# Kernel tuning notes

Hardware: AMD Instinct MI355X
Metric: run time of the kernel (lower is better)

## Reference

```python
import jax, jax.numpy as jnp
import numpy as np

N = 500000   # total nodes in batched graph
B = 8192     # number of graphs
H = 128      # hidden_dim
L = 3        # num_layer -> feature_dim F = H*L = 384
F = H * L
S2S_STEPS = 3
VOCAB = 143


def setup_inputs() -> dict:
    key = jax.random.key(0)
    ks = jax.random.split(key, 12)
    sc = 0.02
    unit_type = jax.random.randint(ks[0], (N,), 0, VOCAB)
    # sorted segment ids covering every graph (contiguous, all B segments non-empty)
    node2graph = (jnp.arange(N) * B) // N
    return {
        'unit_type': unit_type,
        'node2graph': node2graph,
        'embed':    jax.random.normal(ks[1], (VOCAB, H)) * sc,
        'msg_W1':   jax.random.normal(ks[2], (H, 2 * H)) * sc,
        'msg_b1':   jnp.zeros((H,)),
        'msg_W2':   jax.random.normal(ks[3], (H, H)) * sc,
        'msg_b2':   jnp.zeros((H,)),
        'gru_Wih':  jax.random.normal(ks[4], (3 * H, H)) * sc,
        'gru_Whh':  jax.random.normal(ks[5], (3 * H, H)) * sc,
        'gru_bih':  jnp.zeros((3 * H,)),
        'gru_bhh':  jnp.zeros((3 * H,)),
        'lstm_Wih': jax.random.normal(ks[6], (4 * F, 2 * F)) * sc,
        'lstm_Whh': jax.random.normal(ks[7], (4 * F, F)) * sc,
        'lstm_bih': jnp.zeros((4 * F,)),
        'lstm_bhh': jnp.zeros((4 * F,)),
    }


def _gru_step(x, h, Wih, Whh, bih, bhh):
    # single-timestep PyTorch GRU cell; gate order r, z, n
    gi = x @ Wih.T + bih
    gh = h @ Whh.T + bhh
    ir, iz, inn = jnp.split(gi, 3, axis=-1)
    hr, hz, hn = jnp.split(gh, 3, axis=-1)
    r = jax.nn.sigmoid(ir + hr)
    z = jax.nn.sigmoid(iz + hz)
    n = jnp.tanh(inn + r * hn)
    return (1.0 - z) * n + z * h


def _lstm_step(x, h, c, Wih, Whh, bih, bhh):
    # single-timestep PyTorch LSTM cell; gate order i, f, g, o
    g = x @ Wih.T + bih + h @ Whh.T + bhh
    i, f, gc, o = jnp.split(g, 4, axis=-1)
    c = jax.nn.sigmoid(f) * c + jax.nn.sigmoid(i) * jnp.tanh(gc)
    h = jax.nn.sigmoid(o) * jnp.tanh(c)
    return h, c


def reference(unit_type, node2graph, embed, msg_W1, msg_b1, msg_W2, msg_b2,
              gru_Wih, gru_Whh, gru_bih, gru_bhh,
              lstm_Wih, lstm_Whh, lstm_bih, lstm_bhh):
    # --- node update stack ---
    layer_input = embed[unit_type]          # [N, H]
    hx = layer_input                        # GRU hidden state (1 layer)
    hiddens = []
    for _ in range(L):
        x2 = jnp.concatenate([layer_input, layer_input], axis=-1)   # [N, 2H]
        msg = jnp.maximum(x2 @ msg_W1.T + msg_b1, 0.0) @ msg_W2.T + msg_b2
        hx = _gru_step(msg, hx, gru_Wih, gru_Whh, gru_bih, gru_bhh)
        hiddens.append(hx)
        layer_input = hx
    node_feature = jnp.concatenate(hiddens, axis=-1)                # [N, F]

    # --- Set2Set readout ---
    h = jnp.zeros((B, F), dtype=node_feature.dtype)
    c = jnp.zeros((B, F), dtype=node_feature.dtype)
    q_star = jnp.zeros((B, 2 * F), dtype=node_feature.dtype)
    for _ in range(S2S_STEPS):
        h, c = _lstm_step(q_star, h, c, lstm_Wih, lstm_Whh, lstm_bih, lstm_bhh)
        q = h                                                       # [B, F]
        logits = jnp.sum(q[node2graph] * node_feature, axis=-1)     # [N]
        m = jax.ops.segment_max(logits, node2graph, num_segments=B,
                                indices_are_sorted=True)
        e = jnp.exp(logits - m[node2graph])
        z = jax.ops.segment_sum(e, node2graph, num_segments=B,
                                indices_are_sorted=True)
        att = e / z[node2graph]                                     # [N]
        pooled = jax.ops.segment_sum(att[:, None] * node_feature, node2graph,
                                     num_segments=B, indices_are_sorted=True)
        q_star = jnp.concatenate([q, pooled], axis=-1)              # [B, 2F]

    return q_star, node_feature
```

## Files before the change

### kernel.cpp

```cpp
#include <hip/hip_runtime.h>

typedef unsigned short u16;
typedef unsigned int   u32;
typedef u16 bfx8 __attribute__((ext_vector_type(8)));
typedef __bf16 bf16x8 __attribute__((ext_vector_type(8)));
typedef float  f32x4  __attribute__((ext_vector_type(4)));

#define NH  128
#define NF  384
#define K2F 768
#define NG4 1536

__device__ __forceinline__ float bf2f(u16 u){ return __uint_as_float(((u32)u) << 16); }
__device__ __forceinline__ u16 f2bf(float f){
  u32 x = __float_as_uint(f);
  u32 r = x + 0x7fffu + ((x >> 16) & 1u);
  return (u16)(r >> 16);
}
__device__ __forceinline__ float fsig(float x){ return 1.0f / (1.0f + __expf(-x)); }
__device__ __forceinline__ float ftanh(float x){ return 1.0f - 2.0f / (__expf(2.0f * x) + 1.0f); }

struct P {
  const int *unit_type, *n2g;
  const void *embed, *w1, *b1, *w2, *b2, *gwih, *gwhh, *gbih, *gbhh, *lwih, *lwhh, *lbih, *lbhh;
  int *flag, *segS, *segE;
  u16 *W1eb, *W2b, *Wihb, *Whhb;
  float *b1f, *b2f, *bihG, *bhhG;
  float *Wcat;
  float *bsum;
  float *h1v, *c1v;
  float *hbuf, *cbuf, *pooled;
  float *xcat;
  float *gout;
  u16 *nfb;
  int useNfb;
  void *out; long qsz;
  int N, B, embedN;
};

__device__ __forceinline__ float ldin(const void* p, long i, int isbf){
  return isbf ? bf2f(((const u16*)p)[i]) : ((const float*)p)[i];
}

__global__ void k_detect(P p){
  __shared__ int cnt;
  if (threadIdx.x == 0) cnt = 0;
  __syncthreads();
  const u32* w = (const u32*)p.embed;
  const int nw = p.embedN / 2;
  int bad = 0;
  for (int i = threadIdx.x; i < nw; i += blockDim.x){
    u32 v = w[i];
    float fhi = __uint_as_float(v & 0xffff0000u);
    float flo = __uint_as_float(v << 16);
    if (!(fabsf(fhi) < 2.0f)) bad++;
    if (!(fabsf(flo) < 2.0f)) bad++;
  }
  atomicAdd(&cnt, bad);
  __syncthreads();
  if (threadIdx.x == 0) *p.flag = (cnt == 0) ? 1 : 0;
}

__global__ void k_prep(P p){
  long o = (long)blockIdx.x * 256 + threadIdx.x;
  const int isbf = *p.flag;
  if (o < 16384){ long cc = o >> 7, k = o & 127;
    float v = ldin(p.w1, cc*256 + k, isbf) + ldin(p.w1, cc*256 + 128 + k, isbf);
    p.W1eb[o] = f2bf(v); return; } o -= 16384;
  if (o < 16384){ p.W2b[o]  = f2bf(ldin(p.w2, o, isbf));   return; } o -= 16384;
  if (o < 49152){ p.Wihb[o] = f2bf(ldin(p.gwih, o, isbf)); return; } o -= 49152;
  if (o < 49152){ p.Whhb[o] = f2bf(ldin(p.gwhh, o, isbf)); return; } o -= 49152;
  if (o < (long)NG4*K2F){ long j = o / K2F, k = o - j*K2F;
    float v = ldin(p.lwih, o, isbf);
    if (k < NF) v += ldin(p.lwhh, j*NF + k, isbf);
    p.Wcat[o] = v; return; } o -= (long)NG4*K2F;
  if (o < NH){ p.b1f[o] = ldin(p.b1, o, isbf); return; } o -= NH;
  if (o < NH){ p.b2f[o] = ldin(p.b2, o, isbf); return; } o -= NH;
  if (o < NF){ p.bihG[o] = ldin(p.gbih, o, isbf); return; } o -= NF;
  if (o < NF){ p.bhhG[o] = ldin(p.gbhh, o, isbf); return; } o -= NF;
  if (o < NG4){ p.bsum[o] = ldin(p.lbih, o, isbf) + ldin(p.lbhh, o, isbf); return; } o -= NG4;
  if (o < p.B){ p.segS[o] = 0; p.segE[o] = 0; }
}

__global__ void k_segb(P p){
  int i = (int)blockIdx.x * 256 + threadIdx.x;
  if (i >= p.N) return;
  int g = p.n2g[i];
  if (g < 0 || g >= p.B) return;
  if (i == 0        || p.n2g[i-1] != g) p.segS[g] = i;
  if (i == p.N - 1  || p.n2g[i+1] != g) p.segE[g] = i + 1;
}

__device__ __forceinline__ f32x4 MF(bf16x8 a, bf16x8 b, f32x4 c){
  return __builtin_amdgcn_mfma_f32_16x16x32_bf16(a, b, c, 0, 0, 0);
}
__device__ __forceinline__ bf16x8 ldA(const u16* buf, int m0, int k0, int lane){
  const int row = m0 + (lane & 15);
  const int byte = (row*256 + (k0 + (lane>>4)*8)*2) ^ ((row&7)<<4);
  return *(const bf16x8*)((const char*)buf + byte);
}
__device__ __forceinline__ bf16x8 ldB(const u16* __restrict__ W, int n0, int k0, int lane){
  return *(const bf16x8*)(W + (long)(n0 + (lane&15))*NH + k0 + (lane>>4)*8);
}
__device__ __forceinline__ void stLDS(u16* buf, int row, int col, float v){
  const int byte = (row*256 + col*2) ^ ((row&7)<<4);
  *(u16*)((char*)buf + byte) = f2bf(v);
}
__device__ __forceinline__ void stLDSu(u16* buf, int row, int col, u16 v){
  const int byte = (row*256 + col*2) ^ ((row&7)<<4);
  *(u16*)((char*)buf + byte) = v;
}
__device__ __forceinline__ float ldLDS(const u16* buf, int row, int col){
  const int byte = (row*256 + col*2) ^ ((row&7)<<4);
  return bf2f(*(const u16*)((const char*)buf + byte));
}
__device__ __forceinline__ bfx8 ldLDS8(const u16* buf, int row, int col8){
  const int byte = (row*256 + col8*2) ^ ((row&7)<<4);
  return *(const bfx8*)((const char*)buf + byte);
}

__global__ __launch_bounds__(256, 3) void k_stageA_mfma(P p){
  __shared__ u16 hA[64*128];
  __shared__ u16 mA[64*128];
  __shared__ u16 gA[64*128];
  const int t = (int)threadIdx.x;
  const int lane = t & 63, w = t >> 6;
  const int node0 = (int)blockIdx.x * 64;
  const int cL = lane & 15;
  const int isbf = *p.flag;

  u16 st[2][2][4][4];

  {
    const int row = t >> 2, seg = t & 3;
    const int node = min(node0 + row, p.N - 1);
    int ut = p.unit_type[node];
    ut = min(max(ut, 0), p.embedN/NH - 1);
    if (isbf){
      const u16* src = (const u16*)p.embed + (long)ut*NH + seg*32;
      #pragma unroll
      for (int i = 0; i < 4; ++i){
        const int col = seg*32 + i*8;
        const int byte = (row*256 + col*2) ^ ((row&7)<<4);
        *(bfx8*)((char*)hA + byte) = *(const bfx8*)(src + i*8);
      }
    } else {
      const float* src = (const float*)p.embed + (long)ut*NH + seg*32;
      #pragma unroll
      for (int i = 0; i < 4; ++i){
        const int col = seg*32 + i*8;
        u16 tmp[8];
        #pragma unroll
        for (int j = 0; j < 8; ++j) tmp[j] = f2bf(src[i*8 + j]);
        const int byte = (row*256 + col*2) ^ ((row&7)<<4);
        *(bfx8*)((char*)hA + byte) = *(const bfx8*)tmp;
      }
    }
  }
  __syncthreads();

  u16*   out16 = (u16*)p.out;
  float* out32 = (float*)p.out;

  #pragma unroll 1
  for (int l = 0; l < 3; ++l){
    {
      f32x4 acc[2][4];
      #pragma unroll
      for (int nt = 0; nt < 2; ++nt){
        const float b = p.b1f[w*32 + nt*16 + cL];
        #pragma unroll
        for (int m = 0; m < 4; ++m) acc[nt][m] = {b,b,b,b};
      }
      for (int k0 = 0; k0 < 128; k0 += 32){
        bf16x8 a[4];
        #pragma unroll
        for (int m = 0; m < 4; ++m) a[m] = ldA(hA, m*16, k0, lane);
        #pragma unroll
        for (int nt = 0; nt < 2; ++nt){
          const bf16x8 b = ldB(p.W1eb, w*32 + nt*16, k0, lane);
          #pragma unroll
          for (int m = 0; m < 4; ++m) acc[nt][m] = MF(a[m], b, acc[nt][m]);
        }
      }
      #pragma unroll
      for (int nt = 0; nt < 2; ++nt)
        #pragma unroll
        for (int m = 0; m < 4; ++m)
          #pragma unroll
          for (int j = 0; j < 4; ++j)
            stLDS(mA, m*16 + (lane>>4)*4 + j, w*32 + nt*16 + cL,
                  fmaxf(acc[nt][m][j], 0.0f));
    }
    __syncthreads();
    {
      f32x4 acc[2][4];
      #pragma unroll
      for (int nt = 0; nt < 2; ++nt){
        const float b = p.b2f[w*32 + nt*16 + cL];
        #pragma unroll
        for (int m = 0; m < 4; ++m) acc[nt][m] = {b,b,b,b};
      }
      for (int k0 = 0; k0 < 128; k0 += 32){
        bf16x8 a[4];
        #pragma unroll
        for (int m = 0; m < 4; ++m) a[m] = ldA(mA, m*16, k0, lane);
        #pragma unroll
        for (int nt = 0; nt < 2; ++nt){
          const bf16x8 b = ldB(p.W2b, w*32 + nt*16, k0, lane);
          #pragma unroll
          for (int m = 0; m < 4; ++m) acc[nt][m] = MF(a[m], b, acc[nt][m]);
        }
      }
      __syncthreads();
      #pragma unroll
      for (int nt = 0; nt < 2; ++nt)
        #pragma unroll
        for (int m = 0; m < 4; ++m)
          #pragma unroll
          for (int j = 0; j < 4; ++j)
            stLDS(gA, m*16 + (lane>>4)*4 + j, w*32 + nt*16 + cL, acc[nt][m][j]);
    }
    __syncthreads();
    f32x4 rr[2][4];
    {
      f32x4 acc[4][4];
      #pragma unroll
      for (int tc = 0; tc < 4; ++tc){
        const int col = (tc < 2 ? 0 : 128) + w*32 + (tc&1)*16 + cL;
        const float b = p.bihG[col] + p.bhhG[col];
        #pragma unroll
        for (int m = 0; m < 4; ++m) acc[tc][m] = {b,b,b,b};
      }
      for (int k0 = 0; k0 < 128; k0 += 32){
        bf16x8 a[4];
        #pragma unroll
        for (int m = 0; m < 4; ++m) a[m] = ldA(gA, m*16, k0, lane);
        #pragma unroll
        for (int tc = 0; tc < 4; ++tc){
          const bf16x8 b = ldB(p.Wihb, (tc < 2 ? 0 : 128) + w*32 + (tc&1)*16, k0, lane);
          #pragma unroll
          for (int m = 0; m < 4; ++m) acc[tc][m] = MF(a[m], b, acc[tc][m]);
        }
      }
      for (int k0 = 0; k0 < 128; k0 += 32){
        bf16x8 a[4];
        #pragma unroll
        for (int m = 0; m < 4; ++m) a[m] = ldA(hA, m*16, k0, lane);
        #pragma unroll
        for (int tc = 0; tc < 4; ++tc){
          const bf16x8 b = ldB(p.Whhb, (tc < 2 ? 0 : 128) + w*32 + (tc&1)*16, k0, lane);
          #pragma unroll
          for (int m = 0; m < 4; ++m) acc[tc][m] = MF(a[m], b, acc[tc][m]);
        }
      }
      #pragma unroll
      for (int nt = 0; nt < 2; ++nt)
        #pragma unroll
        for (int m = 0; m < 4; ++m)
          #pragma unroll
          for (int j = 0; j < 4; ++j){
            rr[nt][m][j] = fsig(acc[nt][m][j]);
            stLDS(mA, m*16 + (lane>>4)*4 + j, w*32 + nt*16 + cL,
                  fsig(acc[nt+2][m][j]));
          }
    }
    {
      f32x4 inn[2][4], hnn[2][4];
      #pragma unroll
      for (int nt = 0; nt < 2; ++nt){
        const int col = 256 + w*32 + nt*16 + cL;
        const float bi = p.bihG[col], bh = p.bhhG[col];
        #pragma unroll
        for (int m = 0; m < 4; ++m){ inn[nt][m] = {bi,bi,bi,bi}; hnn[nt][m] = {bh,bh,bh,bh}; }
      }
      for (int k0 = 0; k0 < 128; k0 += 32){
        bf16x8 a[4];
        #pragma unroll
        for (int m = 0; m < 4; ++m) a[m] = ldA(gA, m*16, k0, lane);
        #pragma unroll
        for (int nt = 0; nt < 2; ++nt){
          const bf16x8 b = ldB(p.Wihb, 256 + w*32 + nt*16, k0, lane);
          #pragma unroll
          for (int m = 0; m < 4; ++m) inn[nt][m] = MF(a[m], b, inn[nt][m]);
        }
      }
      for (int k0 = 0; k0 < 128; k0 += 32){
        bf16x8 a[4];
        #pragma unroll
        for (int m = 0; m < 4; ++m) a[m] = ldA(hA, m*16, k0, lane);
        #pragma unroll
        for (int nt = 0; nt < 2; ++nt){
          const bf16x8 b = ldB(p.Whhb, 256 + w*32 + nt*16, k0, lane);
          #pragma unroll
          for (int m = 0; m < 4; ++m) hnn[nt][m] = MF(a[m], b, hnn[nt][m]);
        }
      }
      #pragma unroll
      for (int nt = 0; nt < 2; ++nt)
        #pragma unroll
        for (int m = 0; m < 4; ++m)
          #pragma unroll
          for (int j = 0; j < 4; ++j){
            const int row = m*16 + (lane>>4)*4 + j;
            const int col = w*32 + nt*16 + cL;
            const float nn = ftanh(fmaf(rr[nt][m][j], hnn[nt][m][j], inn[nt][m][j]));
            const float zv = ldLDS(mA, row, col);
            const float hv = ldLDS(hA, row, col);
            inn[nt][m][j] = fmaf(zv, hv - nn, nn);
          }
      __syncthreads();
      #pragma unroll
      for (int nt = 0; nt < 2; ++nt)
        #pragma unroll
        for (int m = 0; m < 4; ++m)
          #pragma unroll
          for (int j = 0; j < 4; ++j){
            const u16 hv16 = f2bf(inn[nt][m][j]);
            stLDSu(hA, m*16 + (lane>>4)*4 + j, w*32 + nt*16 + cL, hv16);
            if (l == 0) st[0][nt][m][j] = hv16;
            else if (l == 1) st[1][nt][m][j] = hv16;
          }
      __syncthreads();
    }
  }

  #pragma unroll
  for (int nt = 0; nt < 2; ++nt)
    #pragma unroll
    for (int m = 0; m < 4; ++m)
      #pragma unroll
      for (int j = 0; j < 4; ++j){
        const int row = m*16 + (lane>>4)*4 + j;
        const int col = w*32 + nt*16 + cL;
        stLDSu(mA, row, col, st[0][nt][m][j]);
        stLDSu(gA, row, col, st[1][nt][m][j]);
      }
  __syncthreads();

  {
    const int r0 = t >> 4;
    const int c8 = (t & 15) * 8;
    #pragma unroll
    for (int r4 = 0; r4 < 4; ++r4){
      const int row = r0 + r4*16;
      const int node = node0 + row;
      if (node < p.N){
        const bfx8 v0 = ldLDS8(mA, row, c8);
        const bfx8 v1 = ldLDS8(gA, row, c8);
        const bfx8 v2 = ldLDS8(hA, row, c8);
        const long base = (long)node*NF;
        if (isbf){
          __builtin_nontemporal_store(v0, (bfx8*)(out16 + p.qsz + base + c8));
          __builtin_nontemporal_store(v1, (bfx8*)(out16 + p.qsz + base + NH + c8));
          __builtin_nontemporal_store(v2, (bfx8*)(out16 + p.qsz + base + 2*NH + c8));
        } else {
          #pragma unroll
          for (int lyr = 0; lyr < 3; ++lyr){
            const bfx8 v = lyr == 0 ? v0 : (lyr == 1 ? v1 : v2);
            f32x4 lo, hi;
            #pragma unroll
            for (int j = 0; j < 4; ++j){ lo[j] = bf2f(v[j]); hi[j] = bf2f(v[j+4]); }
            __builtin_nontemporal_store(lo, (f32x4*)(out32 + p.qsz + base + lyr*NH + c8));
            __builtin_nontemporal_store(hi, (f32x4*)(out32 + p.qsz + base + lyr*NH + c8 + 4));
          }
          if (p.useNfb){
            __builtin_nontemporal_store(v0, (bfx8*)(p.nfb + base + c8));
            __builtin_nontemporal_store(v1, (bfx8*)(p.nfb + base + NH + c8));
            __builtin_nontemporal_store(v2, (bfx8*)(p.nfb + base + 2*NH + c8));
          }
        }
      }
    }
  }
}

__global__ void k_lstm0(P p){
  const int d = (int)threadIdx.x;
  if (d >= NF) return;
  const float i_ = fsig(p.bsum[d]);
  const float gc = ftanh(p.bsum[2*NF + d]);
  const float o_ = fsig(p.bsum[3*NF + d]);
  const float cn = i_ * gc;
  p.c1v[d] = cn;
  p.h1v[d] = o_ * ftanh(cn);
}

__global__ __launch_bounds__(256) void k_attn(P p, const float* __restrict__ qsrc,
                                              int qstride, int finalstep){
  __shared__ alignas(16) char raw[32 * NF * 4];
  __shared__ float qs[NF];
  __shared__ float att[32];
  __shared__ float sM, sZ, sSc;

  u16*   nb = (u16*)raw;
  float* nfl = (float*)raw;
  const int t = (int)threadIdx.x;
  const int g = (int)blockIdx.x;
  const int isbf = *p.flag;
  const int bftile = isbf | p.useNfb;
  const u16* nbase = isbf ? (const u16*)p.out + p.qsz : p.nfb;
  const float* o32 = (const float*)p.out;

  for (int i = t; i < NF; i += 256) qs[i] = qsrc[(long)g*qstride + i];
  if (t == 0){ sM = -1e30f; sZ = 0.0f; sSc = 1.0f; }
  int n0 = p.segS[g], n1 = p.segE[g];
  n0 = max(n0, 0); n1 = min(n1, p.N);
  float acc0 = 0.f, acc1 = 0.f;
  __syncthreads();

  for (int base = n0; base < n1; base += 32){
    const int cnt = min(32, n1 - base);
    {
      const int i = t >> 3, q8 = t & 7;
      if (i < cnt){
        if (bftile){
          const bfx8* src = (const bfx8*)(nbase + (long)(base + i)*NF + q8*48);
          #pragma unroll
          for (int j8 = 0; j8 < 6; ++j8)
            *(bfx8*)&nb[i*NF + q8*48 + j8*8] = __builtin_nontemporal_load(src + j8);
        } else {
          const f32x4* src = (const f32x4*)(o32 + p.qsz + (long)(base + i)*NF + q8*48);
          #pragma unroll
          for (int j4 = 0; j4 < 12; ++j4)
            *(f32x4*)&nfl[i*NF + q8*48 + j4*4] = __builtin_nontemporal_load(src + j4);
        }
      }
    }
    __syncthreads();
    {
      const int w = t >> 6, lane = t & 63;
      for (int ii = w; ii < cnt; ii += 4){
        float dot = 0.f;
        #pragma unroll
        for (int j = 0; j < 6; ++j){
          const int d = lane + 64*j;
          const float v = bftile ? bf2f(nb[ii*NF + d]) : nfl[ii*NF + d];
          dot = fmaf(v, qs[d], dot);
        }
        #pragma unroll
        for (int off = 32; off; off >>= 1) dot += __shfl_xor(dot, off);
        if (lane == 0) att[ii] = dot;
      }
    }
    __syncthreads();
    if (t < 32){
      const float l = (t < cnt) ? att[t] : -1e30f;
      float m = l;
      #pragma unroll
      for (int off = 16; off; off >>= 1) m = fmaxf(m, __shfl_xor(m, off));
      const float mnew = fmaxf(sM, m);
      const float e = (t < cnt) ? __expf(l - mnew) : 0.f;
      float z = e;
      #pragma unroll
      for (int off = 16; off; off >>= 1) z += __shfl_xor(z, off);
      if (t < cnt) att[t] = e;
      if (t == 0){
        const float sc = __expf(sM - mnew);
        sSc = sc; sZ = sZ * sc + z; sM = mnew;
      }
    }
    __syncthreads();
    {
      const float sc = sSc;
      acc0 *= sc; acc1 *= sc;
      for (int ii = 0; ii < cnt; ++ii){
        const float a = att[ii];
        const float v0 = bftile ? bf2f(nb[ii*NF + t]) : nfl[ii*NF + t];
        acc0 = fmaf(a, v0, acc0);
        if (t < 128){
          const float v1 = bftile ? bf2f(nb[ii*NF + 256 + t]) : nfl[ii*NF + 256 + t];
          acc1 = fmaf(a, v1, acc1);
        }
      }
    }
    __syncthreads();
  }

  const float invZ = (sZ != 0.0f) ? 1.0f / sZ : 0.0f;
  const float p0 = acc0 * invZ, p1 = acc1 * invZ;
  p.pooled[(long)g*NF + t] = p0;
  if (t < 128) p.pooled[(long)g*NF + 256 + t] = p1;
  if (finalstep){
    const long rb = (long)g * K2F;
    if (isbf){
      u16* o = (u16*)p.out;
      o[rb + t] = f2bf(qs[t]);
      if (t < 128) o[rb + 256 + t] = f2bf(qs[256 + t]);
      o[rb + NF + t] = f2bf(p0);
      if (t < 128) o[rb + NF + 256 + t] = f2bf(p1);
    } else {
      float* o = (float*)p.out;
      o[rb + t] = qs[t];
      if (t < 128) o[rb + 256 + t] = qs[256 + t];
      o[rb + NF + t] = p0;
      if (t < 128) o[rb + NF + 256 + t] = p1;
    }
  }
}

__global__ void k_xcat(P p, const float* __restrict__ hsrc, int hstride){
  const int d2 = (int)blockIdx.x * 256 + threadIdx.x;
  const int g  = (int)blockIdx.y;
  if (d2 >= K2F) return;
  const float v = (d2 < NF) ? hsrc[(long)g*hstride + d2]
                            : p.pooled[(long)g*NF + d2 - NF];
  p.xcat[(long)g*K2F + d2] = v;
}

__global__ __launch_bounds__(256) void k_gemm(P p){
  __shared__ alignas(16) float aT[32][128];
  __shared__ alignas(16) float wT[32][128];
  const int t = (int)threadIdx.x;
  const int tx = t & 15, ty = t >> 4;
  const int row0 = (int)blockIdx.x * 128, col0 = (int)blockIdx.y * 128;
  const int M = p.B;
  float acc[8][8];
  #pragma unroll
  for (int i = 0; i < 8; ++i)
    #pragma unroll
    for (int j = 0; j < 8; ++j) acc[i][j] = 0.f;

  const int r = t >> 1, ks = (t & 1) * 16;
  for (int kc = 0; kc < K2F; kc += 32){
    {
      const int gr = row0 + r;
      float v[16];
      if (gr < M){
        const float* src = p.xcat + (long)gr*K2F + kc + ks;
        *(float4*)&v[0]  = *(const float4*)(src);
        *(float4*)&v[4]  = *(const float4*)(src + 4);
        *(float4*)&v[8]  = *(const float4*)(src + 8);
        *(float4*)&v[12] = *(const float4*)(src + 12);
      } else {
        #pragma unroll
        for (int j = 0; j < 16; ++j) v[j] = 0.f;
      }
      #pragma unroll
      for (int j = 0; j < 16; ++j) aT[ks+j][r] = v[j];
      const float* wsrc = p.Wcat + (long)(col0 + r)*K2F + kc + ks;
      *(float4*)&v[0]  = *(const float4*)(wsrc);
      *(float4*)&v[4]  = *(const float4*)(wsrc + 4);
      *(float4*)&v[8]  = *(const float4*)(wsrc + 8);
      *(float4*)&v[12] = *(const float4*)(wsrc + 12);
      #pragma unroll
      for (int j = 0; j < 16; ++j) wT[ks+j][r] = v[j];
    }
    __syncthreads();
    #pragma unroll 2
    for (int k = 0; k < 32; ++k){
      float a[8], wv[8];
      *(float4*)&a[0]  = *(const float4*)&aT[k][ty*8];
      *(float4*)&a[4]  = *(const float4*)&aT[k][ty*8 + 4];
      *(float4*)&wv[0] = *(const float4*)&wT[k][tx*8];
      *(float4*)&wv[4] = *(const float4*)&wT[k][tx*8 + 4];
      #pragma unroll
      for (int i = 0; i < 8; ++i)
        #pragma unroll
        for (int j = 0; j < 8; ++j) acc[i][j] = fmaf(a[i], wv[j], acc[i][j]);
    }
    __syncthreads();
  }
  float bs[8];
  #pragma unroll
  for (int j = 0; j < 8; ++j) bs[j] = p.bsum[col0 + tx*8 + j];
  #pragma unroll
  for (int i = 0; i < 8; ++i){
    const int gr = row0 + ty*8 + i;
    if (gr < M){
      float* crow = p.gout + (long)gr*NG4 + col0 + tx*8;
      float o[8];
      #pragma unroll
      for (int j = 0; j < 8; ++j) o[j] = acc[i][j] + bs[j];
      *(float4*)&crow[0] = *(const float4*)&o[0];
      *(float4*)&crow[4] = *(const float4*)&o[4];
    }
  }
}

__global__ void k_gates(P p, const float* __restrict__ csrc, int cstride){
  const long idx = (long)blockIdx.x * 256 + threadIdx.x;
  if (idx >= (long)p.B * NF) return;
  const int g = (int)(idx / NF), d = (int)(idx - (long)g*NF);
  const float* gr = p.gout + (long)g*NG4;
  const float i_ = fsig(gr[d]);
  const float f_ = fsig(gr[NF + d]);
  const float gc = ftanh(gr[2*NF + d]);
  const float o_ = fsig(gr[3*NF + d]);
  const float cp = csrc[(long)g*cstride + d];
  const float cn = fmaf(f_, cp, i_ * gc);
  p.cbuf[(long)g*NF + d] = cn;
  p.hbuf[(long)g*NF + d] = o_ * ftanh(cn);
}

extern "C" void kernel_launch(void* const* d_in, const int* in_sizes, int n_in,
                              void* d_out, int out_size, void* d_ws, size_t ws_size,
                              hipStream_t stream){
  P p{};
  p.unit_type = (const int*)d_in[0];
  p.n2g  = (const int*)d_in[1];
  p.embed = d_in[2];  p.w1 = d_in[3];  p.b1 = d_in[4];  p.w2 = d_in[5];  p.b2 = d_in[6];
  p.gwih = d_in[7];  p.gwhh = d_in[8]; p.gbih = d_in[9]; p.gbhh = d_in[10];
  p.lwih = d_in[11]; p.lwhh = d_in[12]; p.lbih = d_in[13]; p.lbhh = d_in[14];

  const int N = in_sizes[0];
  const int B = (int)(((long)out_size - (long)N*NF) / K2F);
  p.N = N; p.B = B; p.embedN = in_sizes[2];
  p.out = d_out; p.qsz = (long)B * K2F;

  char* w = (char*)d_ws;
  size_t used = 0;
  auto alloc = [&](size_t bytes) -> char* {
    char* r = w + used;
    used += (bytes + 255) & ~(size_t)255;
    return r;
  };
  p.flag  = (int*)alloc(4);
  p.segS  = (int*)alloc((size_t)B*4);
  p.segE  = (int*)alloc((size_t)B*4);
  p.W1eb  = (u16*)  alloc(16384*2);
  p.W2b   = (u16*)  alloc(16384*2);
  p.Wihb  = (u16*)  alloc(49152*2);
  p.Whhb  = (u16*)  alloc(49152*2);
  p.b1f   = (float*)alloc(NH*4);
  p.b2f   = (float*)alloc(NH*4);
  p.bihG  = (float*)alloc(NF*4);
  p.bhhG  = (float*)alloc(NF*4);
  p.Wcat  = (float*)alloc((size_t)NG4*K2F*4);
  p.bsum  = (float*)alloc(NG4*4);
  p.h1v   = (float*)alloc(NF*4);
  p.c1v   = (float*)alloc(NF*4);
  p.hbuf  = (float*)alloc((size_t)B*NF*4);
  p.cbuf  = (float*)alloc((size_t)B*NF*4);
  p.pooled= (float*)alloc((size_t)B*NF*4);
  p.xcat  = (float*)alloc((size_t)B*K2F*4);
  p.gout  = (float*)alloc((size_t)B*NG4*4);
  if (used > ws_size){
    (void)hipMemsetAsync(d_out, 0, (size_t)out_size * 2, stream);
    return;
  }
  const size_t nfbBytes = (size_t)N * NF * 2;
  if (used + nfbBytes + 256 <= ws_size){
    p.nfb = (u16*)alloc(nfbBytes);
    p.useNfb = 1;
  } else {
    p.nfb = (u16*)p.flag;
    p.useNfb = 0;
  }

  const long prepTot = 16384 + 16384 + 49152 + 49152
                     + (long)NG4*K2F + NH + NH + NF + NF + NG4 + B;

  k_detect<<<1, 256, 0, stream>>>(p);
  k_prep  <<<(int)((prepTot + 255)/256), 256, 0, stream>>>(p);
  k_segb  <<<(N + 255)/256, 256, 0, stream>>>(p);
  k_stageA_mfma<<<(N + 63)/64, 256, 0, stream>>>(p);
  k_lstm0 <<<1, NF, 0, stream>>>(p);

  const int gemmGx = (B + 127)/128;
  k_attn <<<B, 256, 0, stream>>>(p, p.h1v, 0, 0);
  k_xcat <<<dim3(3, B), 256, 0, stream>>>(p, p.h1v, 0);
  k_gemm <<<dim3(gemmGx, NG4/128), 256, 0, stream>>>(p);
  k_gates<<<(int)(((long)B*NF + 255)/256), 256, 0, stream>>>(p, p.c1v, 0);
  k_attn <<<B, 256, 0, stream>>>(p, p.hbuf, NF, 0);
  k_xcat <<<dim3(3, B), 256, 0, stream>>>(p, p.hbuf, NF);
  k_gemm <<<dim3(gemmGx, NG4/128), 256, 0, stream>>>(p);
  k_gates<<<(int)(((long)B*NF + 255)/256), 256, 0, stream>>>(p, p.cbuf, NF);
  k_attn <<<B, 256, 0, stream>>>(p, p.hbuf, NF, 1);
}
```

Before: 2.373 ms.

## Cut stage-A LDS and registers to raise occupancy, store layers incrementally

```diff
diff --git a/kernel.cpp b/kernel.cpp
--- a/kernel.cpp
+++ b/kernel.cpp
@@ -3,6 +3,7 @@
 typedef unsigned short u16;
 typedef unsigned int   u32;
 typedef u16 bfx8 __attribute__((ext_vector_type(8)));
+typedef u16 bfx4 __attribute__((ext_vector_type(4)));
 typedef __bf16 bf16x8 __attribute__((ext_vector_type(8)));
 typedef float  f32x4  __attribute__((ext_vector_type(4)));
 
@@ -24,6 +25,7 @@
   const int *unit_type, *n2g;
   const void *embed, *w1, *b1, *w2, *b2, *gwih, *gwhh, *gbih, *gbhh, *lwih, *lwhh, *lbih, *lbhh;
   int *flag, *segS, *segE;
+  u16 *embedB;
   u16 *W1eb, *W2b, *Wihb, *Whhb;
   float *b1f, *b2f, *bihG, *bhhG;
   float *Wcat;
@@ -64,6 +66,7 @@
 __global__ void k_prep(P p){
   long o = (long)blockIdx.x * 256 + threadIdx.x;
   const int isbf = *p.flag;
+  if (o < p.embedN){ p.embedB[o] = f2bf(ldin(p.embed, o, isbf)); return; } o -= p.embedN;
   if (o < 16384){ long cc = o >> 7, k = o & 127;
     float v = ldin(p.w1, cc*256 + k, isbf) + ldin(p.w1, cc*256 + 128 + k, isbf);
     p.W1eb[o] = f2bf(v); return; } o -= 16384;
@@ -106,10 +109,6 @@
   const int byte = (row*256 + col*2) ^ ((row&7)<<4);
   *(u16*)((char*)buf + byte) = f2bf(v);
 }
-__device__ __forceinline__ void stLDSu(u16* buf, int row, int col, u16 v){
-  const int byte = (row*256 + col*2) ^ ((row&7)<<4);
-  *(u16*)((char*)buf + byte) = v;
-}
 __device__ __forceinline__ float ldLDS(const u16* buf, int row, int col){
   const int byte = (row*256 + col*2) ^ ((row&7)<<4);
   return bf2f(*(const u16*)((const char*)buf + byte));
@@ -118,43 +117,31 @@
   const int byte = (row*256 + col8*2) ^ ((row&7)<<4);
   return *(const bfx8*)((const char*)buf + byte);
 }
-
-__global__ __launch_bounds__(256, 3) void k_stageA_mfma(P p){
+__device__ __forceinline__ bfx4 ldLDS4(const u16* buf, int row, int col4){
+  const int byte = (row*256 + col4*2) ^ ((row&7)<<4);
+  return *(const bfx4*)((const char*)buf + byte);
+}
+
+__global__ __launch_bounds__(256, 4) void k_stageA_mfma(P p){
   __shared__ u16 hA[64*128];
-  __shared__ u16 mA[64*128];
-  __shared__ u16 gA[64*128];
+  __shared__ u16 mT[64*128];
   const int t = (int)threadIdx.x;
   const int lane = t & 63, w = t >> 6;
   const int node0 = (int)blockIdx.x * 64;
   const int cL = lane & 15;
   const int isbf = *p.flag;
 
-  u16 st[2][2][4][4];
-
   {
     const int row = t >> 2, seg = t & 3;
     const int node = min(node0 + row, p.N - 1);
     int ut = p.unit_type[node];
     ut = min(max(ut, 0), p.embedN/NH - 1);
-    if (isbf){
-      const u16* src = (const u16*)p.embed + (long)ut*NH + seg*32;
-      #pragma unroll
-      for (int i = 0; i < 4; ++i){
-        const int col = seg*32 + i*8;
-        const int byte = (row*256 + col*2) ^ ((row&7)<<4);
-        *(bfx8*)((char*)hA + byte) = *(const bfx8*)(src + i*8);
-      }
-    } else {
-      const float* src = (const float*)p.embed + (long)ut*NH + seg*32;
-      #pragma unroll
-      for (int i = 0; i < 4; ++i){
-        const int col = seg*32 + i*8;
-        u16 tmp[8];
-        #pragma unroll
-        for (int j = 0; j < 8; ++j) tmp[j] = f2bf(src[i*8 + j]);
-        const int byte = (row*256 + col*2) ^ ((row&7)<<4);
-        *(bfx8*)((char*)hA + byte) = *(const bfx8*)tmp;
-      }
+    const u16* src = p.embedB + (long)ut*NH + seg*32;
+    #pragma unroll
+    for (int i = 0; i < 4; ++i){
+      const int col = seg*32 + i*8;
+      const int byte = (row*256 + col*2) ^ ((row&7)<<4);
+      *(bfx8*)((char*)hA + byte) = *(const bfx8*)(src + i*8);
     }
   }
   __syncthreads();
@@ -189,7 +176,7 @@
         for (int m = 0; m < 4; ++m)
           #pragma unroll
           for (int j = 0; j < 4; ++j)
-            stLDS(mA, m*16 + (lane>>4)*4 + j, w*32 + nt*16 + cL,
+            stLDS(mT, m*16 + (lane>>4)*4 + j, w*32 + nt*16 + cL,
                   fmaxf(acc[nt][m][j], 0.0f));
     }
     __syncthreads();
@@ -204,7 +191,7 @@
       for (int k0 = 0; k0 < 128; k0 += 32){
         bf16x8 a[4];
         #pragma unroll
-        for (int m = 0; m < 4; ++m) a[m] = ldA(mA, m*16, k0, lane);
+        for (int m = 0; m < 4; ++m) a[m] = ldA(mT, m*16, k0, lane);
         #pragma unroll
         for (int nt = 0; nt < 2; ++nt){
           const bf16x8 b = ldB(p.W2b, w*32 + nt*16, k0, lane);
@@ -219,28 +206,29 @@
         for (int m = 0; m < 4; ++m)
           #pragma unroll
           for (int j = 0; j < 4; ++j)
-            stLDS(gA, m*16 + (lane>>4)*4 + j, w*32 + nt*16 + cL, acc[nt][m][j]);
-    }
-    __syncthreads();
+            stLDS(mT, m*16 + (lane>>4)*4 + j, w*32 + nt*16 + cL, acc[nt][m][j]);
+    }
+    __syncthreads();
+
     f32x4 rr[2][4];
     {
-      f32x4 acc[4][4];
-      #pragma unroll
-      for (int tc = 0; tc < 4; ++tc){
-        const int col = (tc < 2 ? 0 : 128) + w*32 + (tc&1)*16 + cL;
+      f32x4 acc[2][4];
+      #pragma unroll
+      for (int nt = 0; nt < 2; ++nt){
+        const int col = w*32 + nt*16 + cL;
         const float b = p.bihG[col] + p.bhhG[col];
         #pragma unroll
-        for (int m = 0; m < 4; ++m) acc[tc][m] = {b,b,b,b};
-      }
-      for (int k0 = 0; k0 < 128; k0 += 32){
-        bf16x8 a[4];
-        #pragma unroll
-        for (int m = 0; m < 4; ++m) a[m] = ldA(gA, m*16, k0, lane);
-        #pragma unroll
-        for (int tc = 0; tc < 4; ++tc){
-          const bf16x8 b = ldB(p.Wihb, (tc < 2 ? 0 : 128) + w*32 + (tc&1)*16, k0, lane);
-          #pragma unroll
-          for (int m = 0; m < 4; ++m) acc[tc][m] = MF(a[m], b, acc[tc][m]);
+        for (int m = 0; m < 4; ++m) acc[nt][m] = {b,b,b,b};
+      }
+      for (int k0 = 0; k0 < 128; k0 += 32){
+        bf16x8 a[4];
+        #pragma unroll
+        for (int m = 0; m < 4; ++m) a[m] = ldA(mT, m*16, k0, lane);
+        #pragma unroll
+        for (int nt = 0; nt < 2; ++nt){
+          const bf16x8 b = ldB(p.Wihb, w*32 + nt*16, k0, lane);
+          #pragma unroll
+          for (int m = 0; m < 4; ++m) acc[nt][m] = MF(a[m], b, acc[nt][m]);
         }
       }
       for (int k0 = 0; k0 < 128; k0 += 32){
@@ -248,10 +236,10 @@
         #pragma unroll
         for (int m = 0; m < 4; ++m) a[m] = ldA(hA, m*16, k0, lane);
         #pragma unroll
-        for (int tc = 0; tc < 4; ++tc){
-          const bf16x8 b = ldB(p.Whhb, (tc < 2 ? 0 : 128) + w*32 + (tc&1)*16, k0, lane);
-          #pragma unroll
-          for (int m = 0; m < 4; ++m) acc[tc][m] = MF(a[m], b, acc[tc][m]);
+        for (int nt = 0; nt < 2; ++nt){
+          const bf16x8 b = ldB(p.Whhb, w*32 + nt*16, k0, lane);
+          #pragma unroll
+          for (int m = 0; m < 4; ++m) acc[nt][m] = MF(a[m], b, acc[nt][m]);
         }
       }
       #pragma unroll
@@ -259,41 +247,86 @@
         #pragma unroll
         for (int m = 0; m < 4; ++m)
           #pragma unroll
-          for (int j = 0; j < 4; ++j){
-            rr[nt][m][j] = fsig(acc[nt][m][j]);
-            stLDS(mA, m*16 + (lane>>4)*4 + j, w*32 + nt*16 + cL,
-                  fsig(acc[nt+2][m][j]));
-          }
-    }
-    {
-      f32x4 inn[2][4], hnn[2][4];
+          for (int j = 0; j < 4; ++j) rr[nt][m][j] = fsig(acc[nt][m][j]);
+    }
+    f32x4 zz[2][4];
+    {
+      f32x4 acc[2][4];
       #pragma unroll
       for (int nt = 0; nt < 2; ++nt){
-        const int col = 256 + w*32 + nt*16 + cL;
-        const float bi = p.bihG[col], bh = p.bhhG[col];
-        #pragma unroll
-        for (int m = 0; m < 4; ++m){ inn[nt][m] = {bi,bi,bi,bi}; hnn[nt][m] = {bh,bh,bh,bh}; }
-      }
-      for (int k0 = 0; k0 < 128; k0 += 32){
-        bf16x8 a[4];
-        #pragma unroll
-        for (int m = 0; m < 4; ++m) a[m] = ldA(gA, m*16, k0, lane);
+        const int col = 128 + w*32 + nt*16 + cL;
+        const float b = p.bihG[col] + p.bhhG[col];
+        #pragma unroll
+        for (int m = 0; m < 4; ++m) acc[nt][m] = {b,b,b,b};
+      }
+      for (int k0 = 0; k0 < 128; k0 += 32){
+        bf16x8 a[4];
+        #pragma unroll
+        for (int m = 0; m < 4; ++m) a[m] = ldA(mT, m*16, k0, lane);
+        #pragma unroll
+        for (int nt = 0; nt < 2; ++nt){
+          const bf16x8 b = ldB(p.Wihb, 128 + w*32 + nt*16, k0, lane);
+          #pragma unroll
+          for (int m = 0; m < 4; ++m) acc[nt][m] = MF(a[m], b, acc[nt][m]);
+        }
+      }
+      for (int k0 = 0; k0 < 128; k0 += 32){
+        bf16x8 a[4];
+        #pragma unroll
+        for (int m = 0; m < 4; ++m) a[m] = ldA(hA, m*16, k0, lane);
+        #pragma unroll
+        for (int nt = 0; nt < 2; ++nt){
+          const bf16x8 b = ldB(p.Whhb, 128 + w*32 + nt*16, k0, lane);
+          #pragma unroll
+          for (int m = 0; m < 4; ++m) acc[nt][m] = MF(a[m], b, acc[nt][m]);
+        }
+      }
+      #pragma unroll
+      for (int nt = 0; nt < 2; ++nt)
+        #pragma unroll
+        for (int m = 0; m < 4; ++m)
+          #pragma unroll
+          for (int j = 0; j < 4; ++j) zz[nt][m][j] = fsig(acc[nt][m][j]);
+    }
+    {
+      f32x4 acc[2][4];
+      #pragma unroll
+      for (int nt = 0; nt < 2; ++nt){
+        const float bh = p.bhhG[256 + w*32 + nt*16 + cL];
+        #pragma unroll
+        for (int m = 0; m < 4; ++m) acc[nt][m] = {bh,bh,bh,bh};
+      }
+      for (int k0 = 0; k0 < 128; k0 += 32){
+        bf16x8 a[4];
+        #pragma unroll
+        for (int m = 0; m < 4; ++m) a[m] = ldA(hA, m*16, k0, lane);
+        #pragma unroll
+        for (int nt = 0; nt < 2; ++nt){
+          const bf16x8 b = ldB(p.Whhb, 256 + w*32 + nt*16, k0, lane);
+          #pragma unroll
+          for (int m = 0; m < 4; ++m) acc[nt][m] = MF(a[m], b, acc[nt][m]);
+        }
+      }
+      #pragma unroll
+      for (int nt = 0; nt < 2; ++nt)
+        #pragma unroll
+        for (int m = 0; m < 4; ++m) rr[nt][m] = rr[nt][m] * acc[nt][m];
+
+      #pragma unroll
+      for (int nt = 0; nt < 2; ++nt){
+        const float bi = p.bihG[256 + w*32 + nt*16 + cL];
+        #pragma unroll
+        for (int m = 0; m < 4; ++m) acc[nt][m] = {bi,bi,bi,bi};
+      }
+      for (int k0 = 0; k0 < 128; k0 += 32){
+        bf16x8 a[4];
+        #pragma unroll
+        for (int m = 0; m < 4; ++m) a[m] = ldA(mT, m*16, k0, lane);
         #pragma unroll
         for (int nt = 0; nt < 2; ++nt){
           const bf16x8 b = ldB(p.Wihb, 256 + w*32 + nt*16, k0, lane);
           #pragma unroll
-          for (int m = 0; m < 4; ++m) inn[nt][m] = MF(a[m], b, inn[nt][m]);
-        }
-      }
-      for (int k0 = 0; k0 < 128; k0 += 32){
-        bf16x8 a[4];
-        #pragma unroll
-        for (int m = 0; m < 4; ++m) a[m] = ldA(hA, m*16, k0, lane);
-        #pragma unroll
-        for (int nt = 0; nt < 2; ++nt){
-          const bf16x8 b = ldB(p.Whhb, 256 + w*32 + nt*16, k0, lane);
-          #pragma unroll
-          for (int m = 0; m < 4; ++m) hnn[nt][m] = MF(a[m], b, hnn[nt][m]);
+          for (int m = 0; m < 4; ++m) acc[nt][m] = MF(a[m], b, acc[nt][m]);
         }
       }
       #pragma unroll
@@ -304,10 +337,9 @@
           for (int j = 0; j < 4; ++j){
             const int row = m*16 + (lane>>4)*4 + j;
             const int col = w*32 + nt*16 + cL;
-            const float nn = ftanh(fmaf(rr[nt][m][j], hnn[nt][m][j], inn[nt][m][j]));
-            const float zv = ldLDS(mA, row, col);
+            const float nn = ftanh(rr[nt][m][j] + acc[nt][m][j]);
             const float hv = ldLDS(hA, row, col);
-            inn[nt][m][j] = fmaf(zv, hv - nn, nn);
+            acc[nt][m][j] = fmaf(zz[nt][m][j], hv - nn, nn);
           }
       __syncthreads();
       #pragma unroll
@@ -315,59 +347,34 @@
         #pragma unroll
         for (int m = 0; m < 4; ++m)
           #pragma unroll
-          for (int j = 0; j < 4; ++j){
-            const u16 hv16 = f2bf(inn[nt][m][j]);
-            stLDSu(hA, m*16 + (lane>>4)*4 + j, w*32 + nt*16 + cL, hv16);
-            if (l == 0) st[0][nt][m][j] = hv16;
-            else if (l == 1) st[1][nt][m][j] = hv16;
-          }
+          for (int j = 0; j < 4; ++j)
+            stLDS(hA, m*16 + (lane>>4)*4 + j, w*32 + nt*16 + cL, acc[nt][m][j]);
       __syncthreads();
     }
-  }
-
-  #pragma unroll
-  for (int nt = 0; nt < 2; ++nt)
-    #pragma unroll
-    for (int m = 0; m < 4; ++m)
-      #pragma unroll
-      for (int j = 0; j < 4; ++j){
-        const int row = m*16 + (lane>>4)*4 + j;
-        const int col = w*32 + nt*16 + cL;
-        stLDSu(mA, row, col, st[0][nt][m][j]);
-        stLDSu(gA, row, col, st[1][nt][m][j]);
-      }
-  __syncthreads();
-
-  {
-    const int r0 = t >> 4;
-    const int c8 = (t & 15) * 8;
-    #pragma unroll
-    for (int r4 = 0; r4 < 4; ++r4){
-      const int row = r0 + r4*16;
-      const int node = node0 + row;
-      if (node < p.N){
-        const bfx8 v0 = ldLDS8(mA, row, c8);
-        const bfx8 v1 = ldLDS8(gA, row, c8);
-        const bfx8 v2 = ldLDS8(hA, row, c8);
-        const long base = (long)node*NF;
-        if (isbf){
-          __builtin_nontemporal_store(v0, (bfx8*)(out16 + p.qsz + base + c8));
-          __builtin_nontemporal_store(v1, (bfx8*)(out16 + p.qsz + base + NH + c8));
-          __builtin_nontemporal_store(v2, (bfx8*)(out16 + p.qsz + base + 2*NH + c8));
-        } else {
-          #pragma unroll
-          for (int lyr = 0; lyr < 3; ++lyr){
-            const bfx8 v = lyr == 0 ? v0 : (lyr == 1 ? v1 : v2);
-            f32x4 lo, hi;
+    {
+      const int i16 = t & 15;
+      const int r0  = t >> 4;
+      #pragma unroll
+      for (int r4 = 0; r4 < 4; ++r4){
+        const int row = r0 + r4*16;
+        const int node = node0 + row;
+        if (node < p.N){
+          const long base = (long)node*NF + l*NH;
+          if (isbf){
+            const bfx8 v8 = ldLDS8(hA, row, i16*8);
+            __builtin_nontemporal_store(v8, (bfx8*)(out16 + p.qsz + base + i16*8));
+          } else {
+            const bfx4 va = ldLDS4(hA, row, i16*4);
+            const bfx4 vb = ldLDS4(hA, row, 64 + i16*4);
+            f32x4 fa, fb;
             #pragma unroll
-            for (int j = 0; j < 4; ++j){ lo[j] = bf2f(v[j]); hi[j] = bf2f(v[j+4]); }
-            __builtin_nontemporal_store(lo, (f32x4*)(out32 + p.qsz + base + lyr*NH + c8));
-            __builtin_nontemporal_store(hi, (f32x4*)(out32 + p.qsz + base + lyr*NH + c8 + 4));
-          }
-          if (p.useNfb){
-            __builtin_nontemporal_store(v0, (bfx8*)(p.nfb + base + c8));
-            __builtin_nontemporal_store(v1, (bfx8*)(p.nfb + base + NH + c8));
-            __builtin_nontemporal_store(v2, (bfx8*)(p.nfb + base + 2*NH + c8));
+            for (int j = 0; j < 4; ++j){ fa[j] = bf2f(va[j]); fb[j] = bf2f(vb[j]); }
+            __builtin_nontemporal_store(fa, (f32x4*)(out32 + p.qsz + base + i16*4));
+            __builtin_nontemporal_store(fb, (f32x4*)(out32 + p.qsz + base + 64 + i16*4));
+            if (p.useNfb){
+              const bfx8 v8 = ldLDS8(hA, row, i16*8);
+              __builtin_nontemporal_store(v8, (bfx8*)(p.nfb + base + i16*8));
+            }
           }
         }
       }
@@ -618,6 +625,7 @@
   p.flag  = (int*)alloc(4);
   p.segS  = (int*)alloc((size_t)B*4);
   p.segE  = (int*)alloc((size_t)B*4);
+  p.embedB= (u16*)  alloc((size_t)p.embedN*2);
   p.W1eb  = (u16*)  alloc(16384*2);
   p.W2b   = (u16*)  alloc(16384*2);
   p.Wihb  = (u16*)  alloc(49152*2);
@@ -648,7 +656,7 @@
     p.useNfb = 0;
   }
 
-  const long prepTot = 16384 + 16384 + 49152 + 49152
+  const long prepTot = (long)p.embedN + 16384 + 16384 + 49152 + 49152
                      + (long)NG4*K2F + NH + NH + NF + NF + NG4 + B;
 
   k_detect<<<1, 256, 0, stream>>>(p);
```

New measurement: 4.088 ms. +72.3%, slower.
